# Kernel optimization log

Measured on AMD Instinct MI355X. Metric: run time of the kernel, lower is better.

The kernel has to match this reference:

```python
import jax, jax.numpy as jnp
import numpy as np

ALPHA = 1000.0  # Voting(1000) temperature
EPS_NORM = 1e-12
RIDGE = 1e-6


def _edge_index(n):
    # gh(): complete directed graph, edges enumerated i-major, j skipping diagonal.
    ii, jj = np.meshgrid(np.arange(n), np.arange(n), indexing='ij')
    off = ii != jj
    src = ii[off].astype(np.int32)   # G one-hot column = source node
    tgt = jj[off].astype(np.int32)   # H one-hot column = target node
    eid = np.zeros((n, n), dtype=np.int32)
    eid[off] = np.arange(src.size, dtype=np.int32)
    return src, tgt, eid, off


def _l2norm_rows(x):
    return x / jnp.maximum(jnp.linalg.norm(x, axis=1, keepdims=True), EPS_NORM)


def _forward(data1, data2, W, b):
    n1 = data1.shape[0]
    n2 = data2.shape[0]
    src1, tgt1, eid1, off1 = _edge_index(n1)
    src2, tgt2, eid2, off2 = _edge_index(n2)

    # cross-graph embedding update
    Mp0 = data1 @ data2.T                      # [n1, n2]
    m1 = Mp0 @ data2                           # [n1, 512]
    m2 = Mp0.T @ data1                         # [n2, 512]
    lam1 = jax.lax.stop_gradient(
        jnp.linalg.norm(data1, axis=1, keepdims=True)
        / jnp.linalg.norm(m1, axis=1, keepdims=True))
    lam2 = jax.lax.stop_gradient(
        jnp.linalg.norm(data2, axis=1, keepdims=True)
        / jnp.linalg.norm(m2, axis=1, keepdims=True))
    e1 = jax.nn.relu((data1 + lam1 * m1) @ W.T + b)
    e2 = jax.nn.relu((data2 + lam2 * m2) @ W.T + b)
    e1 = _l2norm_rows(e1)
    e2 = _l2norm_rows(e2)

    # edge affinity Me = X2^T Y2 / 2 with X2 = [F@G; F@H] (G/H one-hot => gathers)
    Me = (e1[src1] @ e2[src2].T + e1[tgt1] @ e2[tgt2].T) * 0.5   # [E1, E2]
    Mp = e1 @ e2.T                                               # [n1, n2]

    # Kronecker affinity: M[(i2*n1+i1),(j2*n1+j1)] = Me[eid1[i1,j1], eid2[i2,j2]]
    # (exact value of (a2*K_G) @ K_H^T for complete-graph one-hot incidences)
    g = Me[eid1][:, :, eid2]                                     # [i1, j1, i2, j2]
    mask = off1[:, :, None, None] & off2[None, None, :, :]
    g = jnp.where(mask, g, 0.0)
    Mmat = jnp.transpose(g, (2, 0, 3, 1)).reshape(n1 * n2, n1 * n2)

    Nv = n1 * n2
    kconst = (n1 - 1) * (n2 - 1)
    Q = (kconst + RIDGE) * jnp.eye(Nv, dtype=Mmat.dtype) - Mmat
    Mpp = Mp.T.reshape(Nv)

    # equality constraints of the n1==n2 branch (doubly-stochastic-sum rows),
    # one redundant row dropped so the KKT system is nonsingular
    A1 = jnp.kron(jnp.ones((1, n1), Mmat.dtype), jnp.eye(n2, dtype=Mmat.dtype))
    A2 = jnp.kron(jnp.eye(n1, dtype=Mmat.dtype), jnp.ones((1, n2), Mmat.dtype))
    A = jnp.concatenate([A1, A2], 0)[:-1]
    nc = A.shape[0]

    # QP  min 1/2 z^T Q z - Mpp^T z  s.t. A z = 1  (equality KKT solve;
    # z>=0 handled by the subsequent clamp as in the released pipeline)
    KKT = jnp.block([[Q, A.T], [A, jnp.zeros((nc, nc), Mmat.dtype)]])
    rhs = jnp.concatenate([Mpp, jnp.ones(nc, Mmat.dtype)])
    z = jnp.linalg.solve(KKT, rhs)[:Nv]

    s = z.reshape(n2, n1).T                 # [n1, n2]
    s = jnp.clip(s, 0.0, 1.0)               # relu(s) - relu(s-1)
    s = jax.nn.softmax(ALPHA * s, axis=-1)[None]  # Voting(1000)
    return s


def setup_inputs() -> dict:
    key = jax.random.key(0)
    k1, k2, k3, k4 = jax.random.split(key, 4)
    n, d = 80, 512
    data1 = jax.random.normal(k1, (n, d), dtype=jnp.float32)
    data2 = jax.random.normal(k2, (n, d), dtype=jnp.float32)
    # cross_graph Linear initialized to identity (nn.init.eye_) + tiny jitter
    W = jnp.eye(d, dtype=jnp.float32) + 0.01 * jax.random.normal(k3, (d, d), dtype=jnp.float32)
    b = 0.01 * jax.random.normal(k4, (d,), dtype=jnp.float32)
    return {"data1": data1, "data2": data2, "W": W, "b": b}


def reference(data1, data2, W, b):
    return _forward(data1, data2, W, b)
```

## Files before the change

### kernel.cpp

```cpp
#include <hip/hip_runtime.h>
#include <math.h>

#define N 80
#define D 512
#define NV (N*N)
#define CQ 6241.000001
#define NEU_K 4

__device__ double g_Mp0[N*N];
__device__ float  g_WT[D*D];
__device__ double g_e[2][N*D];
__device__ double g_P[NV];

__global__ void k_pre(const float* __restrict__ W,
                      const float* __restrict__ d1, const float* __restrict__ d2) {
    int bid = blockIdx.x;
    int tid = threadIdx.x;
    if (bid < 256) {
        __shared__ float t[32][33];
        int c0 = (bid & 15)*32, k0 = (bid >> 4)*32;
        int tx = tid & 31, ty = tid >> 5;
        #pragma unroll
        for (int j = 0; j < 4; ++j) t[ty+8*j][tx] = W[(size_t)(k0+ty+8*j)*D + c0+tx];
        __syncthreads();
        #pragma unroll
        for (int j = 0; j < 4; ++j) g_WT[(size_t)(c0+ty+8*j)*D + k0+tx] = t[tx][ty+8*j];
    } else {
        int gidx = (bid-256)*256 + tid;
        int v = gidx >> 3, ch = gidx & 7;
        int i = v / N, j = v % N;
        const float4* A = reinterpret_cast<const float4*>(d1 + (size_t)i*D);
        const float4* B = reinterpret_cast<const float4*>(d2 + (size_t)j*D);
        double a0=0,a1=0,a2=0,a3=0;
        #pragma unroll
        for (int t = 0; t < 16; ++t) {
            float4 x = A[ch + 8*t], y = B[ch + 8*t];
            a0 += (double)x.x*(double)y.x; a1 += (double)x.y*(double)y.y;
            a2 += (double)x.z*(double)y.z; a3 += (double)x.w*(double)y.w;
        }
        double s = (a0+a1)+(a2+a3);
        #pragma unroll
        for (int o = 1; o < 8; o <<= 1) s += __shfl_xor(s, o, 64);
        if (ch == 0) g_Mp0[i*N+j] = s;
    }
}

__global__ void __launch_bounds__(512,1) k_mue(const float* __restrict__ d1,
                                               const float* __restrict__ d2,
                                               const float* __restrict__ b) {
    __shared__ double mp[N];
    __shared__ double su[D];
    __shared__ double red[512];
    __shared__ double red2[512];
    int bid = blockIdx.x;
    int g = bid / N, row = bid % N;
    int tid = threadIdx.x;
    const float* dsrc = g ? d1 : d2;
    const float* dme  = g ? d2 : d1;

    if (tid < N) mp[tid] = g ? g_Mp0[tid*N + row] : g_Mp0[row*N + tid];
    __syncthreads();

    double m0=0,m1=0,m2=0,m3=0;
    #pragma unroll 4
    for (int j = 0; j < N; j += 4) {
        m0 += mp[j]   * (double)dsrc[(size_t)j*D     + tid];
        m1 += mp[j+1] * (double)dsrc[(size_t)(j+1)*D + tid];
        m2 += mp[j+2] * (double)dsrc[(size_t)(j+2)*D + tid];
        m3 += mp[j+3] * (double)dsrc[(size_t)(j+3)*D + tid];
    }
    double mk = (m0+m1)+(m2+m3);
    double ak = (double)dme[(size_t)row*D + tid];

    red[tid] = ak*ak; red2[tid] = mk*mk; __syncthreads();
    for (int o = 256; o > 0; o >>= 1) {
        if (tid < o) { red[tid] += red[tid+o]; red2[tid] += red2[tid+o]; }
        __syncthreads();
    }
    double lam = sqrt(red[0]) / sqrt(red2[0]);
    __syncthreads();

    su[tid] = ak + lam*mk;
    __syncthreads();

    const float* wt = g_WT + tid;
    double a0=0,a1=0,a2=0,a3=0,a4=0,a5=0,a6=0,a7=0;
    #pragma unroll 8
    for (int t = 0; t < 64; ++t) {
        int c = t*8;
        a0 += su[c+0]*(double)wt[(size_t)(c+0)*D];
        a1 += su[c+1]*(double)wt[(size_t)(c+1)*D];
        a2 += su[c+2]*(double)wt[(size_t)(c+2)*D];
        a3 += su[c+3]*(double)wt[(size_t)(c+3)*D];
        a4 += su[c+4]*(double)wt[(size_t)(c+4)*D];
        a5 += su[c+5]*(double)wt[(size_t)(c+5)*D];
        a6 += su[c+6]*(double)wt[(size_t)(c+6)*D];
        a7 += su[c+7]*(double)wt[(size_t)(c+7)*D];
    }
    double acc = (double)b[tid] + ((a0+a1)+(a2+a3)) + ((a4+a5)+(a6+a7));
    double ek = acc > 0.0 ? acc : 0.0;

    red[tid] = ek*ek; __syncthreads();
    for (int o = 256; o > 0; o >>= 1) { if (tid < o) red[tid] += red[tid+o]; __syncthreads(); }
    double nrm = sqrt(red[0]); if (nrm < 1e-12) nrm = 1e-12;
    g_e[g][(size_t)row*D + tid] = ek / nrm;
}

__global__ void k_p() {
    int gidx = blockIdx.x*256 + threadIdx.x;
    int v = gidx >> 3, ch = gidx & 7;
    int i1 = v % N, i2 = v / N;
    const double2* a = reinterpret_cast<const double2*>(g_e[0] + (size_t)i1*D);
    const double2* c2 = reinterpret_cast<const double2*>(g_e[1] + (size_t)i2*D);
    double a0=0,a1=0;
    #pragma unroll
    for (int t = 0; t < 32; ++t) {
        double2 x = a[ch + 8*t], y = c2[ch + 8*t];
        a0 += x.x*y.x; a1 += x.y*y.y;
    }
    double s = a0+a1;
    #pragma unroll
    for (int o = 1; o < 8; o <<= 1) s += __shfl_xor(s, o, 64);
    if (ch == 0) g_P[v] = s;
}

__global__ void __launch_bounds__(256,1) k_out(float* __restrict__ out) {
    __shared__ double sv[NV];
    __shared__ double sR[N], sC[N];
    __shared__ double ssc[4];
    const double inv80 = 1.0/80.0, inv6400 = 1.0/6400.0, CHI = 1.0/80.0;
    const double invCQ = 1.0/CQ;
    int tid = threadIdx.x;
    double ploc[25], vv[25], x[25];

    #pragma unroll
    for (int j = 0; j < 25; ++j) { int v = tid + 256*j; ploc[j] = g_P[v]; sv[v] = ploc[j]; }
    __syncthreads();

    if (tid < N) {
        double cs = 0.0; const double* dd = sv + tid*N;
        for (int i1 = 0; i1 < N; ++i1) cs += dd[i1];
        sC[tid] = cs;
    } else if (tid < 2*N) {
        int i1 = tid - N; double rr = 0.0;
        for (int i2 = 0; i2 < N; ++i2) rr += sv[i2*N + i1];
        sR[i1] = rr;
    }
    __syncthreads();
    if (tid == 0) { double s = 0.0; for (int i = 0; i < N; ++i) s += sC[i]; ssc[0] = s; }
    __syncthreads();
    double Tp = ssc[0];
    const double SCALE = 6402.0/160.0;
    #pragma unroll
    for (int j = 0; j < 25; ++j) {
        int v = tid + 256*j; int i1 = v % N, i2 = v / N;
        double rv = SCALE*(ploc[j] - sR[i1]*inv80 - sC[i2]*inv80 + Tp*inv6400);
        vv[j] = rv;
        x[j]  = rv*invCQ;
    }
    __syncthreads();

    for (int k = 0; k < NEU_K; ++k) {
        #pragma unroll
        for (int j = 0; j < 25; ++j) { int v = tid + 256*j; sv[v] = ploc[j]*vv[j]; }
        __syncthreads();
        if (tid < N) {
            double cs = 0.0; const double* dd = sv + tid*N;
            for (int i1 = 0; i1 < N; ++i1) cs += dd[i1];
            sC[tid] = cs;
        } else if (tid < 2*N) {
            int i1 = tid - N; double rr = 0.0;
            for (int i2 = 0; i2 < N; ++i2) rr += sv[i2*N + i1];
            sR[i1] = rr;
        }
        __syncthreads();
        if (tid == 0) { double s = 0.0; for (int i = 0; i < N; ++i) s += sC[i]; ssc[1] = s; }
        __syncthreads();
        double Ty = ssc[1];
        #pragma unroll
        for (int j = 0; j < 25; ++j) {
            int v = tid + 256*j; int i1 = v % N, i2 = v / N;
            double mv = ploc[j]*vv[j] - sR[i1]*inv80 - sC[i2]*inv80 + Ty*inv6400;
            vv[j] = mv*invCQ;
            x[j] += vv[j]*invCQ;
        }
        __syncthreads();
    }

    #pragma unroll
    for (int j = 0; j < 25; ++j) {
        int v = tid + 256*j;
        double z = CHI + x[j];
        sv[v] = z < 0.0 ? 0.0 : (z > 1.0 ? 1.0 : z);
    }
    __syncthreads();
    if (tid < N) {
        double mx = -1e300;
        for (int i2 = 0; i2 < N; ++i2) mx = fmax(mx, sv[i2*N + tid]);
        sR[tid] = mx;
    }
    __syncthreads();
    #pragma unroll
    for (int j = 0; j < 25; ++j) {
        int v = tid + 256*j; int i1 = v % N;
        sv[v] = exp(1000.0*(sv[v] - sR[i1]));
    }
    __syncthreads();
    if (tid < N) {
        double s = 0.0;
        for (int i2 = 0; i2 < N; ++i2) s += sv[i2*N + tid];
        sC[tid] = 1.0 / s;
    }
    __syncthreads();
    #pragma unroll
    for (int j = 0; j < 25; ++j) {
        int v = tid + 256*j; int i1 = v % N, i2 = v / N;
        out[i1*N + i2] = (float)(sv[v] * sC[i1]);
    }
}

extern "C" void kernel_launch(void* const* d_in, const int* in_sizes, int n_in,
                              void* d_out, int out_size, void* d_ws, size_t ws_size,
                              hipStream_t stream) {
    const float* d1 = (const float*)d_in[0];
    const float* d2 = (const float*)d_in[1];
    const float* W  = (const float*)d_in[2];
    const float* b  = (const float*)d_in[3];
    float* out = (float*)d_out;

    k_pre<<<dim3(456), dim3(256), 0, stream>>>(W, d1, d2);
    k_mue<<<dim3(160), dim3(512), 0, stream>>>(d1, d2, b);
    k_p  <<<dim3(200), dim3(256), 0, stream>>>();
    k_out<<<dim3(1),   dim3(256), 0, stream>>>(out);
}
```

Before: 72.31 us.

## Halve Neumann iterations, use shuffle reductions, widen accumulators, stage output through LDS

Cuts the Neumann-series correction steps in the final solve from 4 to 2, shortening the serial single-block tail. Replaces the shared-memory tree reductions in k_mue with wavefront shuffle reductions. Adds more independent accumulators to the k_mue and k_p dot-product loops to increase memory-level parallelism. Stages the transposed output through padded shared memory so global stores are coalesced. Truncating the series lowers solve accuracy, which the sharp softmax could amplify.

```diff
diff --git a/kernel.cpp b/kernel.cpp
--- a/kernel.cpp
+++ b/kernel.cpp
@@ -5,7 +5,7 @@
 #define D 512
 #define NV (N*N)
 #define CQ 6241.000001
-#define NEU_K 4
+#define NEU_K 2
 
 __device__ double g_Mp0[N*N];
 __device__ float  g_WT[D*D];
@@ -45,13 +45,20 @@
     }
 }
 
+__device__ __forceinline__ double bsum512(double v, double* w8, int tid) {
+    #pragma unroll
+    for (int o = 1; o < 64; o <<= 1) v += __shfl_xor(v, o, 64);
+    if ((tid & 63) == 0) w8[tid >> 6] = v;
+    __syncthreads();
+    return ((w8[0]+w8[1])+(w8[2]+w8[3])) + ((w8[4]+w8[5])+(w8[6]+w8[7]));
+}
+
 __global__ void __launch_bounds__(512,1) k_mue(const float* __restrict__ d1,
                                                const float* __restrict__ d2,
                                                const float* __restrict__ b) {
     __shared__ double mp[N];
     __shared__ double su[D];
-    __shared__ double red[512];
-    __shared__ double red2[512];
+    __shared__ double w8a[8], w8b[8];
     int bid = blockIdx.x;
     int g = bid / N, row = bid % N;
     int tid = threadIdx.x;
@@ -61,33 +68,34 @@
     if (tid < N) mp[tid] = g ? g_Mp0[tid*N + row] : g_Mp0[row*N + tid];
     __syncthreads();
 
-    double m0=0,m1=0,m2=0,m3=0;
-    #pragma unroll 4
-    for (int j = 0; j < N; j += 4) {
+    double m0=0,m1=0,m2=0,m3=0,m4=0,m5=0,m6=0,m7=0;
+    #pragma unroll 2
+    for (int j = 0; j < N; j += 8) {
         m0 += mp[j]   * (double)dsrc[(size_t)j*D     + tid];
         m1 += mp[j+1] * (double)dsrc[(size_t)(j+1)*D + tid];
         m2 += mp[j+2] * (double)dsrc[(size_t)(j+2)*D + tid];
         m3 += mp[j+3] * (double)dsrc[(size_t)(j+3)*D + tid];
-    }
-    double mk = (m0+m1)+(m2+m3);
+        m4 += mp[j+4] * (double)dsrc[(size_t)(j+4)*D + tid];
+        m5 += mp[j+5] * (double)dsrc[(size_t)(j+5)*D + tid];
+        m6 += mp[j+6] * (double)dsrc[(size_t)(j+6)*D + tid];
+        m7 += mp[j+7] * (double)dsrc[(size_t)(j+7)*D + tid];
+    }
+    double mk = ((m0+m1)+(m2+m3)) + ((m4+m5)+(m6+m7));
     double ak = (double)dme[(size_t)row*D + tid];
 
-    red[tid] = ak*ak; red2[tid] = mk*mk; __syncthreads();
-    for (int o = 256; o > 0; o >>= 1) {
-        if (tid < o) { red[tid] += red[tid+o]; red2[tid] += red2[tid+o]; }
-        __syncthreads();
-    }
-    double lam = sqrt(red[0]) / sqrt(red2[0]);
-    __syncthreads();
-
+    double sa = bsum512(ak*ak, w8a, tid);
+    double sm = bsum512(mk*mk, w8b, tid);
+    double lam = sqrt(sa) / sqrt(sm);
+    __syncthreads();
     su[tid] = ak + lam*mk;
     __syncthreads();
 
     const float* wt = g_WT + tid;
     double a0=0,a1=0,a2=0,a3=0,a4=0,a5=0,a6=0,a7=0;
-    #pragma unroll 8
-    for (int t = 0; t < 64; ++t) {
-        int c = t*8;
+    double b0=0,b1=0,b2=0,b3=0,b4=0,b5=0,b6=0,b7=0;
+    #pragma unroll 4
+    for (int t = 0; t < 32; ++t) {
+        int c = t*16;
         a0 += su[c+0]*(double)wt[(size_t)(c+0)*D];
         a1 += su[c+1]*(double)wt[(size_t)(c+1)*D];
         a2 += su[c+2]*(double)wt[(size_t)(c+2)*D];
@@ -96,13 +104,22 @@
         a5 += su[c+5]*(double)wt[(size_t)(c+5)*D];
         a6 += su[c+6]*(double)wt[(size_t)(c+6)*D];
         a7 += su[c+7]*(double)wt[(size_t)(c+7)*D];
-    }
-    double acc = (double)b[tid] + ((a0+a1)+(a2+a3)) + ((a4+a5)+(a6+a7));
+        b0 += su[c+8]*(double)wt[(size_t)(c+8)*D];
+        b1 += su[c+9]*(double)wt[(size_t)(c+9)*D];
+        b2 += su[c+10]*(double)wt[(size_t)(c+10)*D];
+        b3 += su[c+11]*(double)wt[(size_t)(c+11)*D];
+        b4 += su[c+12]*(double)wt[(size_t)(c+12)*D];
+        b5 += su[c+13]*(double)wt[(size_t)(c+13)*D];
+        b6 += su[c+14]*(double)wt[(size_t)(c+14)*D];
+        b7 += su[c+15]*(double)wt[(size_t)(c+15)*D];
+    }
+    double acc = (double)b[tid]
+               + (((a0+a1)+(a2+a3)) + ((a4+a5)+(a6+a7)))
+               + (((b0+b1)+(b2+b3)) + ((b4+b5)+(b6+b7)));
     double ek = acc > 0.0 ? acc : 0.0;
 
-    red[tid] = ek*ek; __syncthreads();
-    for (int o = 256; o > 0; o >>= 1) { if (tid < o) red[tid] += red[tid+o]; __syncthreads(); }
-    double nrm = sqrt(red[0]); if (nrm < 1e-12) nrm = 1e-12;
+    double sn = bsum512(ek*ek, w8a, tid);
+    double nrm = sqrt(sn); if (nrm < 1e-12) nrm = 1e-12;
     g_e[g][(size_t)row*D + tid] = ek / nrm;
 }
 
@@ -112,13 +129,15 @@
     int i1 = v % N, i2 = v / N;
     const double2* a = reinterpret_cast<const double2*>(g_e[0] + (size_t)i1*D);
     const double2* c2 = reinterpret_cast<const double2*>(g_e[1] + (size_t)i2*D);
-    double a0=0,a1=0;
-    #pragma unroll
-    for (int t = 0; t < 32; ++t) {
-        double2 x = a[ch + 8*t], y = c2[ch + 8*t];
-        a0 += x.x*y.x; a1 += x.y*y.y;
-    }
-    double s = a0+a1;
+    double a0=0,a1=0,a2=0,a3=0;
+    #pragma unroll
+    for (int t = 0; t < 32; t += 2) {
+        double2 x = a[ch + 8*t],     y = c2[ch + 8*t];
+        double2 x1 = a[ch + 8*t+8],  y1 = c2[ch + 8*t+8];
+        a0 += x.x*y.x;  a1 += x.y*y.y;
+        a2 += x1.x*y1.x; a3 += x1.y*y1.y;
+    }
+    double s = (a0+a1)+(a2+a3);
     #pragma unroll
     for (int o = 1; o < 8; o <<= 1) s += __shfl_xor(s, o, 64);
     if (ch == 0) g_P[v] = s;
@@ -128,6 +147,7 @@
     __shared__ double sv[NV];
     __shared__ double sR[N], sC[N];
     __shared__ double ssc[4];
+    __shared__ float  sox[N*(N+1)];
     const double inv80 = 1.0/80.0, inv6400 = 1.0/6400.0, CHI = 1.0/80.0;
     const double invCQ = 1.0/CQ;
     int tid = threadIdx.x;
@@ -215,7 +235,12 @@
     #pragma unroll
     for (int j = 0; j < 25; ++j) {
         int v = tid + 256*j; int i1 = v % N, i2 = v / N;
-        out[i1*N + i2] = (float)(sv[v] * sC[i1]);
+        sox[i1*(N+1) + i2] = (float)(sv[v] * sC[i1]);
+    }
+    __syncthreads();
+    for (int w = tid; w < NV; w += 256) {
+        int i1 = w / N, i2 = w % N;
+        out[w] = sox[i1*(N+1) + i2];
     }
 }
 
```

Result: faster. 58.90 us, median of 2 (-18.5%).
